# Kernel tuning notes

Measured on AMD Instinct MI355X. Metric: run time of the kernel, lower is better.

The kernel has to match this reference:

```python
import jax, jax.numpy as jnp
import numpy as np

B, N, H, HEADS, L = 8, 64, 512, 8, 4
VOCAB, NBOND, CLS = 128, 8, 2
SP = H // HEADS
SCALE = float(np.sqrt(H))  # module divides by sqrt(hidden_dim), not sqrt(sp_dim)


def _ln(x):
    # fresh nn.LayerNorm each call -> gamma=1, beta=0
    m = jnp.mean(x, -1, keepdims=True)
    v = jnp.mean((x - m) ** 2, -1, keepdims=True)
    return (x - m) / jnp.sqrt(v + 1e-5)


def _split(x):  # [B,N,H] -> [B,h,N,sp]
    return x.reshape(B, N, HEADS, SP).transpose(0, 2, 1, 3)


def setup_inputs() -> dict:
    key = jax.random.key(0)
    ks = jax.random.split(key, 16)
    s = 0.05
    return {
        "input_batch": jax.random.randint(ks[0], (B, N), 0, VOCAB),
        "adj_m": jax.random.randint(ks[1], (B, N, N), 0, NBOND),
        "atom_emb": jax.random.normal(ks[2], (VOCAB, H), jnp.float32) * s,
        "bond_emb": jax.random.normal(ks[3], (NBOND, H), jnp.float32) * s,
        "Wq": jax.random.normal(ks[4], (L, H, H), jnp.float32) * s,
        "Wk": jax.random.normal(ks[5], (L, H, H), jnp.float32) * s,
        "Wv": jax.random.normal(ks[6], (L, H, H), jnp.float32) * s,
        "Wew": jax.random.normal(ks[7], (L, H, H), jnp.float32) * s,
        "Wstack": jax.random.normal(ks[8], (L, H, H), jnp.float32) * s,
        "Wf1": jax.random.normal(ks[9], (L, H, 4 * H), jnp.float32) * s,
        "Wf2": jax.random.normal(ks[10], (L, 4 * H, H), jnp.float32) * s,
        "Wout": jax.random.normal(ks[11], (H, H), jnp.float32) * s,
        "Wpred": jax.random.normal(ks[12], (H, CLS), jnp.float32) * s,
        "bpred": jnp.zeros((CLS,), jnp.float32),
    }


def _forward(input_batch, adj_m, atom_emb, bond_emb, Wq, Wk, Wv, Wew,
             Wstack, Wf1, Wf2, Wout, Wpred, bpred):
    x = atom_emb[input_batch]        # [B,N,H] atom embeddings
    bond = bond_emb[adj_m]           # [B,N,N,H] bond embeddings
    neg = jnp.where(adj_m > 0, 0.0, -jnp.inf)[:, None, :, :]  # [B,1,N,N]
    for l in range(L):
        xn = _ln(x)
        q = _split(xn @ Wq[l])
        k = _split(xn @ Wk[l])
        v = _split(xn @ Wv[l])
        ew = bond @ Wew[l]           # [B,N,N,H]
        w = ew.reshape(B, N, N, HEADS, SP).transpose(0, 3, 1, 2, 4)  # [B,h,N,N,sp]
        # bond_influence==1: sim_ij = q_i . (k_j + w_ij)
        logits = jnp.einsum('bhid,bhjd->bhij', q, k) \
               + jnp.einsum('bhid,bhijd->bhij', q, w)
        attn = jax.nn.softmax(logits / SCALE + neg, axis=-1)
        o = jnp.einsum('bhij,bhjd->bhid', attn, v)
        o = o.transpose(0, 2, 1, 3).reshape(B, N, H) @ Wstack[l]
        attn_resid = o + xn
        ff = jax.nn.relu(_ln(attn_resid) @ Wf1[l]) @ Wf2[l]
        x = ff + attn_resid          # transformer_output
        # edge attention update: softmax over {w.w, w.x_i, w.x_j}
        ew_s = jnp.sum(ew * ew, -1)                      # [B,N,N]
        a0 = jnp.einsum('bijh,bih->bij', ew, x)
        a1 = jnp.einsum('bijh,bjh->bij', ew, x)
        wgt = jax.nn.softmax(jnp.stack([ew_s, a0, a1], -1) / SCALE, -1)  # [B,N,N,3]
        bond = (wgt[..., 0:1] * ew
                + wgt[..., 1:2] * x[:, :, None, :]
                + wgt[..., 2:3] * x[:, None, :, :])      # new edge state
    cls = jnp.tanh(x[:, 0, :] @ Wout)
    return jax.nn.softmax(cls @ Wpred + bpred, axis=-1)


def reference(input_batch, adj_m, atom_emb, bond_emb, Wq, Wk, Wv, Wew,
              Wstack, Wf1, Wf2, Wout, Wpred, bpred):
    return _forward(input_batch, adj_m, atom_emb, bond_emb, Wq, Wk, Wv, Wew,
                    Wstack, Wf1, Wf2, Wout, Wpred, bpred)
```

## Files before the change

### kernel.cpp

```cpp
#include <hip/hip_runtime.h>
#include <hip/hip_bf16.h>

typedef __hip_bfloat16 bf16;

#define B_     8
#define N_     64
#define H_     512
#define HEADS_ 8
#define SP_    64
#define L_     4
static constexpr float INV_SCALE = 0.044194173824159216f;

typedef __attribute__((ext_vector_type(8))) short short8;
typedef __attribute__((ext_vector_type(4))) float f32x4;

__device__ __forceinline__ void unpack8(uint4 u, float* f) {
    f[0] = __uint_as_float(u.x << 16); f[1] = __uint_as_float(u.x & 0xffff0000u);
    f[2] = __uint_as_float(u.y << 16); f[3] = __uint_as_float(u.y & 0xffff0000u);
    f[4] = __uint_as_float(u.z << 16); f[5] = __uint_as_float(u.z & 0xffff0000u);
    f[6] = __uint_as_float(u.w << 16); f[7] = __uint_as_float(u.w & 0xffff0000u);
}

__device__ __forceinline__ bf16 f2bf(float v) { return __float2bfloat16(v); }

// ... 84 lines not shown
                    float v = acc[mt][nt][i];
                    if (EPI == 2) v = fmaxf(v, 0.0f);
                    C[(size_t)row * N + col] = __float2bfloat16(v);
                }
            }
    }
}

template <int EPI, bool SPLIT>
__launch_bounds__(256)
__global__ void mfma_gemm_s(const bf16* __restrict__ A, const bf16* __restrict__ Bt,
                            void* __restrict__ Cv, const float* __restrict__ R,
                            int M, int N, int K) {
    __shared__ __align__(16) char lds[4 * 64 * RSTR];
    int kbeg = 0, kend = K;
    const bf16* B2 = Bt;
    void* C2 = Cv;
    if (SPLIT) {
        int ks = K / gridDim.z;
        kbeg = blockIdx.z * ks;
        kend = kbeg + ks;
        C2 = (void*)((float*)Cv + (size_t)blockIdx.z * M * N);
        gemm64_body<0>(lds, A, B2, C2, nullptr, M, N, K, blockIdx.x, blockIdx.y, kbeg, kend);
    } else {
        B2 = Bt + (size_t)blockIdx.z * N * K;
        if (EPI <= 1) C2 = (void*)((float*)Cv + (size_t)blockIdx.z * M * N);
        gemm64_body<EPI>(lds, A, B2, C2, R, M, N, K, blockIdx.x, blockIdx.y, kbeg, kend);
    }
}


__device__ __forceinline__ void ptable_body(char* lds, const float* __restrict__ q,
        const bf16* __restrict__ Bt, float* __restrict__ P, int b, int h, bool shr) {
    char* As = lds;
    char* Bs = lds + 2 * 64 * RSTR;
    const int tid = threadIdx.x;
    const int w = tid >> 6, lane = tid & 63;
    const int wr = (w >> 1) * 32, wc = (w & 1) * 32;
    const int m0 = lane & 15, q4 = lane >> 4;
    const int rA = tid >> 3;
    const int cA = tid & 7;
    const int ksP = cA >> 2;
    const int cB = (cA & 3) * 16;
    const int cE = cA * 8;

    const float* Aq = q + (size_t)(b * 64) * 512 + h * 64;
    const bf16*  Bb = Bt + (shr ? (size_t)0 : (size_t)b * 64 * 512) + h * 64;

    float4 fa0 = *(const float4*)(Aq + (size_t)rA * 512 + cE);
    float4 fa1 = *(const float4*)(Aq + (size_t)rA * 512 + cE + 4);
    float4 fb0 = *(const float4*)(Aq + (size_t)(rA + 32) * 512 + cE);
    float4 fb1 = *(const float4*)(Aq + (size_t)(rA + 32) * 512 + cE + 4);
    uint4 bv0 = *(const uint4*)(Bb + (size_t)rA * 512 + cE);
    uint4 bv1 = *(const uint4*)(Bb + (size_t)(rA + 32) * 512 + cE);
    uint4 av0 = pack8bf(fa0, fa1);
    uint4 av1 = pack8bf(fb0, fb1);
    *(uint4*)(As + ksP * (64 * RSTR) + rA * RSTR + cB) = av0;
    *(uint4*)(As + ksP * (64 * RSTR) + (rA + 32) * RSTR + cB) = av1;
    *(uint4*)(Bs + ksP * (64 * RSTR) + rA * RSTR + cB) = bv0;
    *(uint4*)(Bs + ksP * (64 * RSTR) + (rA + 32) * RSTR + cB) = bv1;
    __syncthreads();

    f32x4 acc[2][2] = {};
    short8 af[2][2], bfr[2][2];
    #pragma unroll
    for (int ks = 0; ks < 2; ++ks)
        #pragma unroll
        for (int t = 0; t < 2; ++t) {
            af[ks][t]  = *(const short8*)(As + ks * (64 * RSTR) + (wr + t * 16 + m0) * RSTR + q4 * 16);
            bfr[ks][t] = *(const short8*)(Bs + ks * (64 * RSTR) + (wc + t * 16 + m0) * RSTR + q4 * 16);
        }
    #pragma unroll
    for (int ks = 0; ks < 2; ++ks)
        #pragma unroll
        for (int mt = 0; mt < 2; ++mt)
            #pragma unroll
            for (int nt = 0; nt < 2; ++nt)
                acc[mt][nt] = __builtin_amdgcn_mfma_f32_16x16x32_bf16(
                    af[ks][mt], bfr[ks][nt], acc[mt][nt], 0, 0, 0);

    #pragma unroll
    for (int mt = 0; mt < 2; ++mt)
        #pragma unroll
        for (int i = 0; i < 4; ++i) {
            int row = wr + mt * 16 + q4 * 4 + i;
            #pragma unroll
            for (int nt = 0; nt < 2; ++nt) {
                int col = wc + nt * 16 + m0;
                P[(((size_t)b * 8 + h) * 64 + row) * 64 + col] = acc[mt][nt][i];
            }
        }
}

__device__ __forceinline__ void ugemm_body(char* lds, const float* __restrict__ q,
        const bf16* __restrict__ wc3, bf16* __restrict__ ubf, int h, int mb, int nb) {
    char* As = lds;
    char* Bs = lds + 2 * 64 * RSTR;
    const int tid = threadIdx.x;
    const int w = tid >> 6, lane = tid & 63;
    const int wr = (w >> 1) * 32, wc = (w & 1) * 32;
    const int m0 = lane & 15, q4 = lane >> 4;
    const int rA = tid >> 3;
    const int cA = tid & 7;
    const int ksP = cA >> 2;
    const int cB = (cA & 3) * 16;
    const int cE = cA * 8;

    const float* Aq = q + (size_t)(mb * 64) * 512 + h * 64;
    const bf16*  Bt = wc3 + (size_t)(nb * 64) * 512 + h * 64;

    float4 fa0 = *(const float4*)(Aq + (size_t)rA * 512 + cE);
    float4 fa1 = *(const float4*)(Aq + (size_t)rA * 512 + cE + 4);
    float4 fb0 = *(const float4*)(Aq + (size_t)(rA + 32) * 512 + cE);
    float4 fb1 = *(const float4*)(Aq + (size_t)(rA + 32) * 512 + cE + 4);
    uint4 b0 = *(const uint4*)(Bt + (size_t)rA * 512 + cE);
    uint4 b1 = *(const uint4*)(Bt + (size_t)(rA + 32) * 512 + cE);
    uint4 a0 = pack8bf(fa0, fa1);
    uint4 a1 = pack8bf(fb0, fb1);
    *(uint4*)(As + ksP * (64 * RSTR) + rA * RSTR + cB) = a0;
    *(uint4*)(As + ksP * (64 * RSTR) + (rA + 32) * RSTR + cB) = a1;
    *(uint4*)(Bs + ksP * (64 * RSTR) + rA * RSTR + cB) = b0;
    *(uint4*)(Bs + ksP * (64 * RSTR) + (rA + 32) * RSTR + cB) = b1;
    __syncthreads();

    f32x4 acc[2][2] = {};
    short8 af[2][2], bfr[2][2];
    #pragma unroll
    for (int ks = 0; ks < 2; ++ks)
        #pragma unroll
        for (int t = 0; t < 2; ++t) {
            af[ks][t]  = *(const short8*)(As + ks * (64 * RSTR) + (wr + t * 16 + m0) * RSTR + q4 * 16);
            bfr[ks][t] = *(const short8*)(Bs + ks * (64 * RSTR) + (wc + t * 16 + m0) * RSTR + q4 * 16);
        }
    #pragma unroll
    for (int ks = 0; ks < 2; ++ks)
        #pragma unroll
        for (int mt = 0; mt < 2; ++mt)
            #pragma unroll
            for (int nt = 0; nt < 2; ++nt)
                acc[mt][nt] = __builtin_amdgcn_mfma_f32_16x16x32_bf16(
                    af[ks][mt], bfr[ks][nt], acc[mt][nt], 0, 0, 0);

    #pragma unroll
    for (int mt = 0; mt < 2; ++mt)
        #pragma unroll
        for (int i = 0; i < 4; ++i) {
            int row = mb * 64 + wr + mt * 16 + q4 * 4 + i;
            #pragma unroll
            for (int nt = 0; nt < 2; ++nt) {
                int col = nb * 64 + wc + nt * 16 + m0;
                ubf[(size_t)row * 4096 + h * 512 + col] = f2bf(acc[mt][nt][i]);
            }
        }
}

__device__ __forceinline__ void coeff1_body(const int* __restrict__ adj,
        const float* __restrict__ c0a, const float* __restrict__ c1a, const float* __restrict__ c2a,
        const float* __restrict__ gbuf, int row, int j,
        float* __restrict__ w0o, float* __restrict__ w1o, float* __restrict__ w2o) {
    int b = row >> 6, i = row & 63;
    int p = row * 64 + j;
    int t = adj[p];
    const float* TXX = gbuf + 0 * 32768 + (size_t)b * 4096;
    const float* TEX = gbuf + 1 * 32768 + (size_t)b * 4096;
    const float* TXx = gbuf + 2 * 32768 + (size_t)b * 4096;
    const float* TEx = gbuf + 3 * 32768 + (size_t)b * 4096;
    const float* TEE = gbuf + 4 * 32768 + (size_t)b * 4096;
    float c0 = c0a[p], c1 = c1a[p], c2 = c2a[p];
    float s1 = c0 * TEx[t * 64 + i] + c1 * TXx[i * 64 + i] + c2 * TXx[j * 64 + i];
    float s2 = c0 * TEx[t * 64 + j] + c1 * TXx[i * 64 + j] + c2 * TXx[j * 64 + j];
    float s0 = c0 * c0 * TEE[t * 64 + t] + c1 * c1 * TXX[i * 64 + i] + c2 * c2 * TXX[j * 64 + j]
             + 2.f * c0 * c1 * TEX[t * 64 + i] + 2.f * c0 * c2 * TEX[t * 64 + j]
             + 2.f * c1 * c2 * TXX[i * 64 + j];
    float t0 = s0 * INV_SCALE, t1 = s1 * INV_SCALE, t2 = s2 * INV_SCALE;
    float m = fmaxf(t0, fmaxf(t1, t2));
    float e0 = expf(t0 - m), e1 = expf(t1 - m), e2 = expf(t2 - m);
    float inv = 1.0f / (e0 + e1 + e2);
    w0o[p] = e0 * inv;
    w1o[p] = e1 * inv;
    w2o[p] = e2 * inv;
}

__device__ __forceinline__ void coeff2_body(const int* __restrict__ adj,
        const float* __restrict__ c0a, const float* __restrict__ c1a, const float* __restrict__ c2a,
        const float* __restrict__ c0b, const float* __restrict__ c1b, const float* __restrict__ c2b,
        const float* __restrict__ gbuf, int row, int j,
        float* __restrict__ w0o, float* __restrict__ w1o, float* __restrict__ w2o) {
    int b = row >> 6, i = row & 63;
    int p = row * 64 + j;
    int t = adj[p];
    const float* TXX = gbuf + 0 * 32768 + (size_t)b * 4096;
    const float* TXY = gbuf + 1 * 32768 + (size_t)b * 4096;
    const float* TYY = gbuf + 2 * 32768 + (size_t)b * 4096;
    const float* TEX = gbuf + 3 * 32768 + (size_t)b * 4096;
    const float* TEY = gbuf + 4 * 32768 + (size_t)b * 4096;
    const float* TEE = gbuf + 5 * 32768 + (size_t)b * 4096;
    const float* TXx = gbuf + 6 * 32768 + (size_t)b * 4096;
    const float* TYx = gbuf + 7 * 32768 + (size_t)b * 4096;
    const float* TEx = gbuf + 8 * 32768 + (size_t)b * 4096;
    float a0 = c0b[p];
    float AE = a0 * c0a[p], Aa = a0 * c1a[p], Ab = a0 * c2a[p];
    float Ac = c1b[p], Ad = c2b[p];
    float s1 = AE * TEx[t * 64 + i] + Aa * TXx[i * 64 + i] + Ab * TXx[j * 64 + i]
             + Ac * TYx[i * 64 + i] + Ad * TYx[j * 64 + i];
    float s2 = AE * TEx[t * 64 + j] + Aa * TXx[i * 64 + j] + Ab * TXx[j * 64 + j]
             + Ac * TYx[i * 64 + j] + Ad * TYx[j * 64 + j];
    float s0 = AE * AE * TEE[t * 64 + t] + Aa * Aa * TXX[i * 64 + i] + Ab * Ab * TXX[j * 64 + j]
             + Ac * Ac * TYY[i * 64 + i] + Ad * Ad * TYY[j * 64 + j]
             + 2.f * AE * Aa * TEX[t * 64 + i] + 2.f * AE * Ab * TEX[t * 64 + j]
             + 2.f * AE * Ac * TEY[t * 64 + i] + 2.f * AE * Ad * TEY[t * 64 + j]
             + 2.f * Aa * Ab * TXX[i * 64 + j]
             + 2.f * Aa * Ac * TXY[i * 64 + i] + 2.f * Aa * Ad * TXY[i * 64 + j]
             + 2.f * Ab * Ac * TXY[j * 64 + i] + 2.f * Ab * Ad * TXY[j * 64 + j]
             + 2.f * Ac * Ad * TYY[i * 64 + j];
    float t0 = s0 * INV_SCALE, t1 = s1 * INV_SCALE, t2 = s2 * INV_SCALE;
    float m = fmaxf(t0, fmaxf(t1, t2));
    float e0 = expf(t0 - m), e1 = expf(t1 - m), e2 = expf(t2 - m);
    float inv = 1.0f / (e0 + e1 + e2);
    w0o[p] = e0 * inv;
    w1o[p] = e1 * inv;
    w2o[p] = e2 * inv;
}

__launch_bounds__(256)
__global__ void setup_kernel(const int* __restrict__ ids, const float* __restrict__ atom_emb,
                             const float* __restrict__ bond_emb,
                             const float* __restrict__ Wq, const float* __restrict__ Wk,
                             const float* __restrict__ Wv, const float* __restrict__ Wew,
                             const float* __restrict__ Wst,
                             const float* __restrict__ Wf1, const float* __restrict__ Wf2,
                             float* __restrict__ xn, bf16* __restrict__ xn_bf,
                             bf16* __restrict__ qkvt, bf16* __restrict__ ewt,
                             bf16* __restrict__ stackt,
                             bf16* __restrict__ f1t, bf16* __restrict__ f2t,
                             bf16* __restrict__ bond_bf, bf16* __restrict__ wc3) {
    __shared__ __align__(16) float smem[64 * 65];
    const size_t KN = (size_t)H_ * H_;
    int bid = blockIdx.x;
    int tid = threadIdx.x;

    if (bid < 512) {
        int row = bid;
        const float* r = atom_emb + (size_t)ids[row] * H_;
        float x0 = r[tid], x1 = r[tid + 256];
        float s = x0 + x1, sq = x0 * x0 + x1 * x1;
        #pragma unroll
        for (int off = 32; off; off >>= 1) {
            s  += __shfl_xor(s,  off);
            sq += __shfl_xor(sq, off);
        }
        int w = tid >> 6;
        if ((tid & 63) == 0) { smem[w] = s; smem[4 + w] = sq; }
        __syncthreads();
        float S = smem[0] + smem[1] + smem[2] + smem[3];
        float Q = smem[4] + smem[5] + smem[6] + smem[7];
        float mean = S * (1.0f / H_);
        float var  = Q * (1.0f / H_) - mean * mean;
        float inv  = rsqrtf(var + 1e-5f);
        float y0 = (x0 - mean) * inv, y1 = (x1 - mean) * inv;
        xn[(size_t)row * H_ + tid]       = y0;
        xn[(size_t)row * H_ + tid + 256] = y1;
        xn_bf[(size_t)row * H_ + tid]       = f2bf(y0);
        xn_bf[(size_t)row * H_ + tid + 256] = f2bf(y1);
    } else if (bid < 3840) {
        const float* W; bf16* Wt; int K, N, kb, nb;
        if (bid < 1792) {
            int idx = bid - 512;
            int z = idx >> 6, rem = idx & 63;
            kb = rem & 7; nb = rem >> 3;
            K = 512; N = 512;
            if (z < 12) {
                int sss = z >> 2, l = z & 3;
                W  = (sss == 0 ? Wq : sss == 1 ? Wk : Wv) + (size_t)l * KN;
                Wt = qkvt + (size_t)l * 3 * KN + (size_t)sss * KN;
            } else if (z < 16) {
                int l = z - 12;
                W = Wew + (size_t)l * KN; Wt = ewt + (size_t)l * KN;
            } else {
                int l = z - 16;
                W = Wst + (size_t)l * KN; Wt = stackt + (size_t)l * KN;
            }
        } else {
            int idx = bid - 1792;
            int z = idx >> 8;
            int idx2 = idx & 255;
            const size_t KN4 = (size_t)4 * H_ * H_;
            if (z < 4) {
                W = Wf1 + (size_t)z * KN4; Wt = f1t + (size_t)z * KN4; K = 512; N = 2048;
                kb = idx2 & 7; nb = idx2 >> 3;
            } else {
                W = Wf2 + (size_t)(z - 4) * KN4; Wt = f2t + (size_t)(z - 4) * KN4; K = 2048; N = 512;
                kb = idx2 >> 3; nb = idx2 & 7;
            }
        }
        int k0 = kb * 64, n0 = nb * 64;
        float (*tt)[65] = (float(*)[65])smem;
        int rr = tid >> 4, c4 = (tid & 15) * 4;
        #pragma unroll
        for (int it = 0; it < 4; ++it) {
            float4 v = *(const float4*)(W + (size_t)(k0 + rr + it * 16) * N + n0 + c4);
            tt[rr + it * 16][c4 + 0] = v.x;
            tt[rr + it * 16][c4 + 1] = v.y;
            tt[rr + it * 16][c4 + 2] = v.z;
            tt[rr + it * 16][c4 + 3] = v.w;
        }
        __syncthreads();
        int nr = tid >> 3, k8 = (tid & 7) * 8;
        #pragma unroll
        for (int it = 0; it < 2; ++it) {
            int nn = nr + it * 32;
            __align__(16) bf16 ob[8];
            #pragma unroll
            for (int e = 0; e < 8; ++e)
                ob[e] = f2bf(tt[k8 + e][nn]);
            *(uint4*)(Wt + (size_t)(n0 + nn) * K + k0 + k8) = *(const uint4*)ob;
        }
    } else if (bid < 3968) {
        int idx = bid - 3840;
        int t = idx >> 1;
        int c = (idx & 1) * 256 + tid;
        bond_bf[t * 512 + c] = (t < 8) ? f2bf(bond_emb[t * 512 + c]) : f2bf(0.0f);
    } else {
        int idx = bid - 3968;
        int gid = idx * 256 + tid;
        const float4* p = (const float4*)(Wew + 3 * KN + (size_t)gid * 8);
        float4 a = p[0], b = p[1];
        *(uint4*)(wc3 + (size_t)gid * 8) = pack8bf(a, b);
    }
}

__launch_bounds__(256)
__global__ void qkv0_e0(const bf16* __restrict__ xn_bf, const bf16* __restrict__ qkvt,
                        float* __restrict__ qkv,
                        const bf16* __restrict__ bond_bf, const bf16* __restrict__ ewt0,
                        bf16* __restrict__ E0) {
    __shared__ __align__(16) char lds[4 * 64 * RSTR];
    int bid = blockIdx.x;
    if (bid < 192) {
        int z = bid >> 6, rem = bid & 63;
        int mb = rem >> 3, by = rem & 7;
        gemm64_body<0>(lds, xn_bf, qkvt + (size_t)z * 262144,
                       qkv + (size_t)z * 262144, nullptr, 512, 512, 512, mb, by, 0, 512);
    } else {
        gemm64_body<3>(lds, bond_bf, ewt0, E0, nullptr, 64, 512, 512,
                       0, bid - 192, 0, 512);
    }
}

__launch_bounds__(256)
__global__ void basis1_qkv_ec(const bf16* __restrict__ x_bf, const bf16* __restrict__ E0,
                              const bf16* __restrict__ ewt1,
                              bf16* __restrict__ xw1, bf16* __restrict__ e0w1,
                              const bf16* __restrict__ xn_bf, const bf16* __restrict__ qkvt_l,
                              float* __restrict__ qkv,
                              const int* __restrict__ adj, const float* __restrict__ x,
                              float* __restrict__ w0o, float* __restrict__ w1o,
                              float* __restrict__ w2o) {
    __shared__ __align__(16) char lds[4 * 64 * RSTR];
    int bid = blockIdx.x;
    if (bid < 264) {
        int bx = bid >> 3, by = bid & 7;
        if (bx < 8)
            gemm64_body<3>(lds, x_bf, ewt1, xw1, nullptr, 512, 512, 512, bx, by, 0, 512);
        else if (bx == 8)
            gemm64_body<3>(lds, E0, ewt1, e0w1, nullptr, 64, 512, 512, 0, by, 0, 512);
        else {
            int tq = bx - 9;
            int z = tq >> 3, mb = tq & 7;
            gemm64_body<0>(lds, xn_bf, qkvt_l + (size_t)z * 262144,
                           qkv + (size_t)z * 262144, nullptr, 512, 512, 512, mb, by, 0, 512);
        }
    } else {
        int k = bid - 264;
        int tid = threadIdx.x;
        int lane = tid & 63, tyv = tid >> 6;
        for (int pp = 0; pp < 4; ++pp) {
            int pair = k * 16 + pp * 4 + tyv;
            int b = pair >> 12;
            int i = (pair >> 6) & 63;
            int j = pair & 63;
            const uint4*  e4  = (const uint4*)(E0 + (size_t)adj[pair] * H_);
            const float4* xi4 = (const float4*)(x + (size_t)(b * 64 + i) * H_);
            const float4* xj4 = (const float4*)(x + (size_t)(b * 64 + j) * H_);
            uint4  eu = e4[lane];
            float4 a0 = xi4[lane * 2], a1 = xi4[lane * 2 + 1];
            float4 c0 = xj4[lane * 2], c1 = xj4[lane * 2 + 1];
            float ef[8], af[8], cf[8];
            unpack8(eu, ef);
            af[0] = a0.x; af[1] = a0.y; af[2] = a0.z; af[3] = a0.w;
            af[4] = a1.x; af[5] = a1.y; af[6] = a1.z; af[7] = a1.w;
            cf[0] = c0.x; cf[1] = c0.y; cf[2] = c0.z; cf[3] = c0.w;
            cf[4] = c1.x; cf[5] = c1.y; cf[6] = c1.z; cf[7] = c1.w;
            float s0 = 0.f, s1 = 0.f, s2 = 0.f;
            #pragma unroll
            for (int t = 0; t < 8; ++t) {
                s0 += ef[t] * ef[t]; s1 += ef[t] * af[t]; s2 += ef[t] * cf[t];
            }
            #pragma unroll
            for (int off = 32; off; off >>= 1) {
                s0 += __shfl_xor(s0, off);
                s1 += __shfl_xor(s1, off);
                s2 += __shfl_xor(s2, off);
            }
            float t0 = s0 * INV_SCALE, t1 = s1 * INV_SCALE, t2 = s2 * INV_SCALE;
            float m = fmaxf(t0, fmaxf(t1, t2));
            float e0 = expf(t0 - m), e1 = expf(t1 - m), e2 = expf(t2 - m);
            float inv = 1.0f / (e0 + e1 + e2);
            if (lane == 0) {
                w0o[pair] = e0 * inv;
                w1o[pair] = e1 * inv;
                w2o[pair] = e2 * inv;
            }
        }
    }
}

__launch_bounds__(256)
__global__ void basis2_qkv_g1(const bf16* __restrict__ xw1, const bf16* __restrict__ x_bf,
                              const bf16* __restrict__ e0w1, const bf16* __restrict__ ewt2,
                              bf16* __restrict__ xw12, bf16* __restrict__ x2w2,
                              bf16* __restrict__ e0w12,
                              const bf16* __restrict__ xn_bf, const bf16* __restrict__ qkvt_l,
                              float* __restrict__ qkv, float* __restrict__ gbuf) {
    __shared__ __align__(16) char lds[4 * 64 * RSTR];
    int bid = blockIdx.x;
    if (bid < 328) {
        int bx = bid >> 3, by = bid & 7;
        if (bx < 8)
            gemm64_body<3>(lds, xw1, ewt2, xw12, nullptr, 512, 512, 512, bx, by, 0, 512);
        else if (bx < 16)
            gemm64_body<3>(lds, x_bf, ewt2, x2w2, nullptr, 512, 512, 512, bx - 8, by, 0, 512);
        else if (bx == 16)
            gemm64_body<3>(lds, e0w1, ewt2, e0w12, nullptr, 64, 512, 512, 0, by, 0, 512);
        else {
            int tq = bx - 17;
            int z = tq >> 3, mb = tq & 7;
            gemm64_body<0>(lds, xn_bf, qkvt_l + (size_t)z * 262144,
                           qkv + (size_t)z * 262144, nullptr, 512, 512, 512, mb, by, 0, 512);
        }
    } else {
        int k = bid - 328;
        int b = k & 7, z = k >> 3;
        size_t ob = (size_t)b * 32768;
        const bf16 *A, *Bt;
        switch (z) {
            case 0: A = xw1 + ob; Bt = xw1 + ob; break;
            case 1: A = e0w1;     Bt = xw1 + ob; break;
            case 2: A = xw1 + ob; Bt = x_bf + ob; break;
            case 3: A = e0w1;     Bt = x_bf + ob; break;
            default: A = e0w1;    Bt = e0w1;     break;
        }
        float* C = gbuf + (size_t)z * 32768 + (size_t)b * 4096;
        gemm64_body<0>(lds, A, Bt, C, nullptr, 64, 64, 512, 0, 0, 0, 512);
    }
}

__launch_bounds__(256)
__global__ void ptable2c(const float* __restrict__ q,
                         const bf16* __restrict__ B0, const bf16* __restrict__ B1,
                         const bf16* __restrict__ B2,
                         float* __restrict__ P0, float* __restrict__ P1,
                         float* __restrict__ P2,
                         const int* __restrict__ adj,
                         const float* __restrict__ c0a, const float* __restrict__ c1a,
                         const float* __restrict__ c2a, const float* __restrict__ gbuf,
                         float* __restrict__ w0o, float* __restrict__ w1o,
                         float* __restrict__ w2o) {
    __shared__ __align__(16) char lds[4 * 64 * RSTR];
    int bid = blockIdx.x;
    if (bid < 192) {
        int z = bid >> 6, rem = bid & 63;
        int b = rem >> 3, h = rem & 7;
        const bf16* Bt = (z == 0) ? B0 : (z == 1 ? B1 : B2);
        float* P = (z == 0) ? P0 : (z == 1 ? P1 : P2);
        ptable_body(lds, q, Bt, P, b, h, z == 2);
    } else {
        int k = bid - 192;
        int tid = threadIdx.x;
        int j = tid & 63;
        #pragma unroll
        for (int pass = 0; pass < 2; ++pass) {
            int row = k * 8 + pass * 4 + (tid >> 6);
            coeff1_body(adj, c0a, c1a, c2a, gbuf, row, j, w0o, w1o, w2o);
        }
    }
}

__launch_bounds__(256)
__global__ void ptable_kernel(const float* __restrict__ q,
                              const bf16* __restrict__ B0, const bf16* __restrict__ B1,
                              float* __restrict__ P0, float* __restrict__ P1) {
    __shared__ __align__(16) char lds[4 * 64 * RSTR];
    const int b = blockIdx.x, h = blockIdx.y, z = blockIdx.z;
    const bf16* Bt = (z == 0) ? B0 : B1;
    float* P = (z == 0) ? P0 : P1;
    ptable_body(lds, q, Bt, P, b, h, z == 1);
}

__launch_bounds__(256)
__global__ void l3qkv_g2(const bf16* __restrict__ xn_bf, const bf16* __restrict__ qkvt_l,
                         float* __restrict__ qkv,
                         const bf16* __restrict__ xw12, const bf16* __restrict__ x2w2,
                         const bf16* __restrict__ e0w12, const bf16* __restrict__ x_bf,
                         float* __restrict__ gbuf) {
    __shared__ __align__(16) char lds[4 * 64 * RSTR];
    int bid = blockIdx.x;
    if (bid < 192) {
        int z = bid >> 6, rem = bid & 63;
        int mb = rem >> 3, by = rem & 7;
        gemm64_body<0>(lds, xn_bf, qkvt_l + (size_t)z * 262144,
                       qkv + (size_t)z * 262144, nullptr, 512, 512, 512, mb, by, 0, 512);
    } else {
        int k = bid - 192;
        int b = k & 7, z = k >> 3;
        size_t ob = (size_t)b * 32768;
        const bf16 *A, *Bt;
        switch (z) {
            case 0: A = xw12 + ob; Bt = xw12 + ob; break;
            case 1: A = xw12 + ob; Bt = x2w2 + ob; break;
            case 2: A = x2w2 + ob; Bt = x2w2 + ob; break;
            case 3: A = e0w12;     Bt = xw12 + ob; break;
            case 4: A = e0w12;     Bt = x2w2 + ob; break;
            case 5: A = e0w12;     Bt = e0w12;     break;
            case 6: A = xw12 + ob; Bt = x_bf + ob; break;
            case 7: A = x2w2 + ob; Bt = x_bf + ob; break;
            default: A = e0w12;    Bt = x_bf + ob; break;
        }
        float* C = gbuf + (size_t)z * 32768 + (size_t)b * 4096;
        gemm64_body<0>(lds, A, Bt, C, nullptr, 64, 64, 512, 0, 0, 0, 512);
    }
}

__launch_bounds__(256)
__global__ void u_c2(const float* __restrict__ q, const bf16* __restrict__ wc3,
                     bf16* __restrict__ ubf,
                     const int* __restrict__ adj,
                     const float* __restrict__ c0a, const float* __restrict__ c1a,
                     const float* __restrict__ c2a,
                     const float* __restrict__ c0b, const float* __restrict__ c1b,
                     const float* __restrict__ c2b,
                     const float* __restrict__ gbuf,
                     float* __restrict__ w0o, float* __restrict__ w1o,
                     float* __restrict__ w2o) {
    __shared__ __align__(16) char lds[4 * 64 * RSTR];
    int bid = blockIdx.x;
    if (bid < 512) {
        int h = bid >> 6, mb = (bid >> 3) & 7, nb = bid & 7;
        ugemm_body(lds, q, wc3, ubf, h, mb, nb);
    } else {
        int k = bid - 512;
        int tid = threadIdx.x;
        int j = tid & 63;
        #pragma unroll
        for (int pass = 0; pass < 2; ++pass) {
            int row = k * 8 + pass * 4 + (tid >> 6);
            coeff2_body(adj, c0a, c1a, c2a, c0b, c1b, c2b, gbuf, row, j, w0o, w1o, w2o);
        }
    }
}

__launch_bounds__(256)
__global__ void mbuf_gemm(const bf16* __restrict__ ubf, const bf16* __restrict__ xw12,
                          const bf16* __restrict__ x2w2, const bf16* __restrict__ x_bf,
                          const bf16* __restrict__ e0w12,
                          float* __restrict__ MX, float* __restrict__ MY,
                          float* __restrict__ MZ, float* __restrict__ DE) {
    __shared__ __align__(16) char lds[4 * 64 * RSTR];
    int b = blockIdx.x, mt = blockIdx.y, z = blockIdx.z;
    const bf16* A = ubf + (size_t)b * 512 * 512;
    const bf16* Bt;
    float* C;
    if (z == 0)      { Bt = xw12 + (size_t)b * 64 * 512; C = MX + (size_t)b * 512 * 64; }
    else if (z == 1) { Bt = x2w2 + (size_t)b * 64 * 512; C = MY + (size_t)b * 512 * 64; }
    else if (z == 2) { Bt = x_bf + (size_t)b * 64 * 512; C = MZ + (size_t)b * 512 * 64; }
    else             { Bt = e0w12;                        C = DE + (size_t)b * 512 * 64; }
    gemm64_body<0>(lds, A, Bt, C, nullptr, 512, 64, 512, mt, 0, 0, 512);
}

__global__ void reduce_stack_ln(const float* __restrict__ part, const float* __restrict__ base,
                                float* __restrict__ resid, bf16* __restrict__ ffin_bf) {
    const int MN = 512 * H_;
    int row = blockIdx.x;
    int tid = threadIdx.x;
    size_t b0 = (size_t)row * H_;
    float v0 = base[b0 + tid], v1 = base[b0 + tid + 256];
    #pragma unroll
    for (int s = 0; s < 4; ++s) {
        v0 += part[(size_t)s * MN + b0 + tid];
        v1 += part[(size_t)s * MN + b0 + tid + 256];
    }
    resid[b0 + tid] = v0;
    resid[b0 + tid + 256] = v1;
    float s = v0 + v1, sq = v0 * v0 + v1 * v1;
    #pragma unroll
    for (int off = 32; off; off >>= 1) {
        s  += __shfl_xor(s,  off);
        sq += __shfl_xor(sq, off);
    }
    __shared__ float ls[4], lq[4];
    int w = tid >> 6;
    if ((tid & 63) == 0) { ls[w] = s; lq[w] = sq; }
    __syncthreads();
    float S = ls[0] + ls[1] + ls[2] + ls[3];
    float Q = lq[0] + lq[1] + lq[2] + lq[3];
    float mean = S * (1.0f / H_);
    float var  = Q * (1.0f / H_) - mean * mean;
    float inv  = rsqrtf(var + 1e-5f);
    ffin_bf[b0 + tid]       = f2bf((v0 - mean) * inv);
    ffin_bf[b0 + tid + 256] = f2bf((v1 - mean) * inv);
}

template <bool DO_LN>
__global__ void reduce_ln_kernel(const float* __restrict__ part, const float* __restrict__ resid,
                                 float* __restrict__ x, bf16* __restrict__ x_bf,
                                 float* __restrict__ xn, bf16* __restrict__ xn_bf) {
    const int MN = 512 * H_;
    int row = blockIdx.x;
    int tid = threadIdx.x;
    size_t base = (size_t)row * H_;
    float v0 = resid[base + tid], v1 = resid[base + tid + 256];
    #pragma unroll
    for (int s = 0; s < 4; ++s) {
        v0 += part[(size_t)s * MN + base + tid];
        v1 += part[(size_t)s * MN + base + tid + 256];
    }
    x[base + tid] = v0;
    x[base + tid + 256] = v1;
    x_bf[base + tid]       = f2bf(v0);
    x_bf[base + tid + 256] = f2bf(v1);
    if (DO_LN) {
        float s = v0 + v1, sq = v0 * v0 + v1 * v1;
        #pragma unroll
        for (int off = 32; off; off >>= 1) {
            s  += __shfl_xor(s,  off);
            sq += __shfl_xor(sq, off);
        }
        __shared__ float ls[4], lq[4];
        int w = tid >> 6;
        if ((tid & 63) == 0) { ls[w] = s; lq[w] = sq; }
        __syncthreads();
        float S = ls[0] + ls[1] + ls[2] + ls[3];
        float Q = lq[0] + lq[1] + lq[2] + lq[3];
        float mean = S * (1.0f / H_);
        float var  = Q * (1.0f / H_) - mean * mean;
        float inv  = rsqrtf(var + 1e-5f);
        float y0 = (v0 - mean) * inv, y1 = (v1 - mean) * inv;
        xn[base + tid]       = y0;
        xn[base + tid + 256] = y1;
        xn_bf[base + tid]       = f2bf(y0);
// ... 167 lines not shown
    for (int off = 32; off; off >>= 1) m = fmaxf(m, __shfl_xor(m, off));
    float pe = expf(logit - m);
    float s = pe;
    #pragma unroll
    for (int off = 32; off; off >>= 1) s += __shfl_xor(s, off);
    as[ty][lane] = pe / s;
    __syncthreads();

    const float* vbase = v + (size_t)(b * 64) * H_ + h * 64;
    float oacc = 0.f;
    int d = lane;
    #pragma unroll 8
    for (int jj = 0; jj < 64; ++jj)
        oacc += as[ty][jj] * vbase[(size_t)jj * H_ + d];
    o[(size_t)bi * H_ + h * 64 + d] = __float2bfloat16(oacc);
}

__global__ void cls_part_kernel(const float* __restrict__ x, const float* __restrict__ Wout,
                                float* __restrict__ clspart) {
    int b  = blockIdx.x;
    int cb = blockIdx.y;
    int ks = blockIdx.z;
    int tid = threadIdx.x;
    int c  = cb * 64 + (tid & 63);
    int kk = tid >> 6;
    const float* xr = x + (size_t)(b * 64) * H_;
    int h0 = ks * 128 + kk * 32;
    float acc = 0.f;
    #pragma unroll
    for (int h = 0; h < 32; ++h)
        acc += xr[h0 + h] * Wout[(size_t)(h0 + h) * H_ + c];
    __shared__ float red[4][64];
    red[kk][tid & 63] = acc;
    __syncthreads();
    if (tid < 64) {
        float v = red[0][tid] + red[1][tid] + red[2][tid] + red[3][tid];
        clspart[((size_t)ks * 8 + b) * H_ + cb * 64 + tid] = v;
    }
}

__global__ void cls_pred2_kernel(const float* __restrict__ clspart,
                                 const float* __restrict__ Wpred,
                                 const float* __restrict__ bpred,
                                 float* __restrict__ out) {
    int b = blockIdx.x;
    int tid = threadIdx.x;
    __shared__ float red0[4], red1[4];
    float a0 = 0.f, a1 = 0.f;
    #pragma unroll
    for (int t = 0; t < 2; ++t) {
        int c = tid + t * 256;
        float v = clspart[((size_t)0 * 8 + b) * H_ + c]
                + clspart[((size_t)1 * 8 + b) * H_ + c]
                + clspart[((size_t)2 * 8 + b) * H_ + c]
                + clspart[((size_t)3 * 8 + b) * H_ + c];
        float tv = tanhf(v);
        a0 += tv * Wpred[c * 2 + 0];
        a1 += tv * Wpred[c * 2 + 1];
    }
    #pragma unroll
    for (int off = 32; off; off >>= 1) {
        a0 += __shfl_xor(a0, off);
        a1 += __shfl_xor(a1, off);
    }
    int w = tid >> 6;
    if ((tid & 63) == 0) { red0[w] = a0; red1[w] = a1; }
    __syncthreads();
    if (tid == 0) {
        float s0 = red0[0] + red0[1] + red0[2] + red0[3] + bpred[0];
        float s1 = red1[0] + red1[1] + red1[2] + red1[3] + bpred[1];
        float m = fmaxf(s0, s1);
        float e0 = expf(s0 - m), e1 = expf(s1 - m);
        float inv = 1.0f / (e0 + e1);
        out[b * 2 + 0] = e0 * inv;
        out[b * 2 + 1] = e1 * inv;
    }
}

extern "C" void kernel_launch(void* const* d_in, const int* in_sizes, int n_in,
                              void* d_out, int out_size, void* d_ws, size_t ws_size,
                              hipStream_t stream) {
    const int*   ids      = (const int*)d_in[0];
    const int*   adj      = (const int*)d_in[1];
    const float* atom_emb = (const float*)d_in[2];
    const float* bond_emb = (const float*)d_in[3];
    const float* Wq     = (const float*)d_in[4];
    const float* Wk     = (const float*)d_in[5];
    const float* Wv     = (const float*)d_in[6];
    const float* Wew    = (const float*)d_in[7];
    const float* Wstack = (const float*)d_in[8];
    const float* Wf1    = (const float*)d_in[9];
    const float* Wf2    = (const float*)d_in[10];
    const float* Wout   = (const float*)d_in[11];
    const float* Wpred  = (const float*)d_in[12];
    const float* bpred  = (const float*)d_in[13];

    char* ws = (char*)d_ws;
    size_t off = 0;
    auto alloc = [&](size_t bytes) {
        size_t o = off;
        off += (bytes + 255) & ~(size_t)255;
        return o;
    };
    const size_t ROWS  = (size_t)B_ * N_;
    const size_t PAIRS = (size_t)B_ * N_ * N_;
    const size_t KN    = (size_t)H_ * H_;

    float* x       = (float*)(ws + alloc(ROWS * H_ * 4));
    float* xn      = (float*)(ws + alloc(ROWS * H_ * 4));
    bf16*  xn_bf   = (bf16*) (ws + alloc(ROWS * H_ * 2));
    bf16*  x_bf    = (bf16*) (ws + alloc(ROWS * H_ * 2));
    float* qkv     = (float*)(ws + alloc(3 * ROWS * H_ * 4));
    bf16*  o_bf    = (bf16*) (ws + alloc(ROWS * H_ * 2));
    float* resid   = (float*)(ws + alloc(ROWS * H_ * 4));
    bf16*  ffin_bf = (bf16*) (ws + alloc(ROWS * H_ * 2));
    bf16*  ffh_bf  = (bf16*) (ws + alloc(ROWS * 4 * H_ * 2));
    float* part    = (float*)(ws + alloc(4 * ROWS * H_ * 4));
    float* clspart = (float*)(ws + alloc(4 * 8 * H_ * 4));
    bf16*  ubf     = (bf16*) (ws + alloc(ROWS * 8 * 512 * 2));
    float* MX      = (float*)(ws + alloc((size_t)4096 * 64 * 4));
    float* MY      = (float*)(ws + alloc((size_t)4096 * 64 * 4));
    float* MZ      = (float*)(ws + alloc((size_t)4096 * 64 * 4));
    float* DE      = (float*)(ws + alloc((size_t)4096 * 64 * 4));
    float* PT0     = (float*)(ws + alloc((size_t)4096 * 64 * 4));
    float* PT1     = (float*)(ws + alloc((size_t)4096 * 64 * 4));
    float* PT2     = (float*)(ws + alloc((size_t)4096 * 64 * 4));
    float* gbuf    = (float*)(ws + alloc((size_t)9 * 8 * 4096 * 4));
    bf16*  wc3     = (bf16*) (ws + alloc(KN * 2));
    bf16*  bond_bf = (bf16*) (ws + alloc(64 * H_ * 2));
    bf16*  E0      = (bf16*) (ws + alloc(64 * H_ * 2));
    bf16*  e0w1    = (bf16*) (ws + alloc(64 * H_ * 2));
    bf16*  e0w12   = (bf16*) (ws + alloc(64 * H_ * 2));
    bf16*  xw1     = (bf16*) (ws + alloc(KN * 2));
    bf16*  xw12    = (bf16*) (ws + alloc(KN * 2));
    bf16*  x2w2    = (bf16*) (ws + alloc(KN * 2));
    float* cw      = (float*)(ws + alloc(9 * PAIRS * 4));
    bf16*  qkvt    = (bf16*) (ws + alloc((size_t)L_ * 3 * KN * 2));
    bf16*  ewt     = (bf16*) (ws + alloc((size_t)L_ * KN * 2));
    bf16*  stackt  = (bf16*) (ws + alloc((size_t)L_ * KN * 2));
    bf16*  f1t     = (bf16*) (ws + alloc((size_t)L_ * 4 * KN * 2));
    bf16*  f2t     = (bf16*) (ws + alloc((size_t)L_ * 4 * KN * 2));
    (void)ws_size;

    float* cw0a = cw;
    float* cw1a = cw + PAIRS;
    float* cw2a = cw + 2 * PAIRS;
    float* cw0b = cw + 3 * PAIRS;
    float* cw1b = cw + 4 * PAIRS;
    float* cw2b = cw + 5 * PAIRS;
    float* cw0c = cw + 6 * PAIRS;
    float* cw1c = cw + 7 * PAIRS;
    float* cw2c = cw + 8 * PAIRS;

    setup_kernel<<<4096, 256, 0, stream>>>(ids, atom_emb, bond_emb,
                                           Wq, Wk, Wv, Wew, Wstack, Wf1, Wf2,
                                           xn, xn_bf, qkvt, ewt, stackt, f1t, f2t,
                                           bond_bf, wc3);

    for (int l = 0; l < L_; ++l) {
        if (l == 0) {
            qkv0_e0<<<200, 256, 0, stream>>>(xn_bf, qkvt, qkv, bond_bf, ewt, E0);
            attn_kernel<true><<<dim3(512, 2), dim3(64, 4), 0, stream>>>(qkv, E0, adj, o_bf);
        } else if (l == 1) {
            basis1_qkv_ec<<<2312, 256, 0, stream>>>(
                x_bf, E0, ewt + KN, xw1, e0w1, xn_bf, qkvt + (size_t)3 * KN, qkv,
                adj, x, cw0a, cw1a, cw2a);
            ptable_kernel<<<dim3(8, 8, 2), 256, 0, stream>>>(qkv, xw1, e0w1, PT0, PT1);
            attn13_kernel<1><<<dim3(512, 2), dim3(64, 4), 0, stream>>>(
                qkv, adj, cw0a, cw1a, cw2a, nullptr, nullptr, nullptr,
                PT0, nullptr, PT1, o_bf);
        } else if (l == 2) {
            basis2_qkv_g1<<<368, 256, 0, stream>>>(
                xw1, x_bf, e0w1, ewt + 2 * KN, xw12, x2w2, e0w12,
                xn_bf, qkvt + (size_t)6 * KN, qkv, gbuf);
            ptable2c<<<256, 256, 0, stream>>>(
                qkv, xw12, x2w2, e0w12, PT0, PT1, PT2,
                adj, cw0a, cw1a, cw2a, gbuf, cw0b, cw1b, cw2b);
            attn13_kernel<2><<<dim3(512, 2), dim3(64, 4), 0, stream>>>(
                qkv, adj, cw0a, cw1a, cw2a, cw0b, cw1b, cw2b,
                PT0, PT1, PT2, o_bf);
        } else {
            l3qkv_g2<<<264, 256, 0, stream>>>(
                xn_bf, qkvt + (size_t)9 * KN, qkv, xw12, x2w2, e0w12, x_bf, gbuf);
            u_c2<<<576, 256, 0, stream>>>(
                qkv, wc3, ubf, adj, cw0a, cw1a, cw2a, cw0b, cw1b, cw2b,
                gbuf, cw0c, cw1c, cw2c);
            mbuf_gemm<<<dim3(8, 8, 4), 256, 0, stream>>>(ubf, xw12, x2w2, x_bf, e0w12,
                                                         MX, MY, MZ, DE);
            attn3s2_kernel<<<dim3(512, 2), dim3(64, 4), 0, stream>>>(
                qkv, adj, cw0a, cw1a, cw2a, cw0b, cw1b, cw2b, cw0c, cw1c, cw2c,
                MX, MY, MZ, DE, o_bf);
        }

        mfma_gemm_s<0, true><<<dim3(8, 8, 4), 256, 0, stream>>>(
            o_bf, stackt + (size_t)l * KN, part, nullptr, 512, 512, 512);
        reduce_stack_ln<<<512, 256, 0, stream>>>(part, xn, resid, ffin_bf);
        mfma_gemm_s<2, false><<<dim3(8, 32), 256, 0, stream>>>(
            ffin_bf, f1t + (size_t)l * 4 * KN, ffh_bf, nullptr, 512, 2048, 512);
        mfma_gemm_s<0, true><<<dim3(8, 8, 4), 256, 0, stream>>>(
            ffh_bf, f2t + (size_t)l * 4 * KN, part, nullptr, 512, 512, 2048);
        if (l < L_ - 1)
            reduce_ln_kernel<true><<<512, 256, 0, stream>>>(part, resid, x, x_bf, xn, xn_bf);
        else
            reduce_ln_kernel<false><<<512, 256, 0, stream>>>(part, resid, x, x_bf, xn, xn_bf);
    }

    cls_part_kernel<<<dim3(8, 8, 4), 256, 0, stream>>>(x, Wout, clspart);
    cls_pred2_kernel<<<8, 256, 0, stream>>>(clspart, Wpred, bpred, (float*)d_out);
}
```

Baseline: 345.9 us.

## Compute layer-1 edge softmax coefficients from small Gram tables instead of per-pair dots

The layer-1 edge-update coefficients were computed by a 2048-block path that, for every (b,i,j) pair, took 512-wide dot products of the bond embedding with itself and with x_i and x_j. Those dots now come from small Gram tables: E0·x per batch and E0·E0 across the bond types, built as extra 64x64 GEMM blocks in the basis/QKV kernel. A lightweight coeff0 pass merged into the ptable launch looks them up. Separately, each setup weight-transpose block now handles two tiles, cutting the setup grid from 4096 to 2432 blocks. The trade-off is an added dependency on gbuf Gram results and bf16 Gram products in place of fp32 dot products.

```diff
diff --git a/kernel.cpp b/kernel.cpp
--- a/kernel.cpp
+++ b/kernel.cpp
@@ -260,6 +260,26 @@
                 ubf[(size_t)row * 4096 + h * 512 + col] = f2bf(acc[mt][nt][i]);
             }
         }
+}
+
+__device__ __forceinline__ void coeff0_body(const int* __restrict__ adj,
+        const float* __restrict__ gbuf, int row, int j,
+        float* __restrict__ w0o, float* __restrict__ w1o, float* __restrict__ w2o) {
+    int b = row >> 6, i = row & 63;
+    int p = row * 64 + j;
+    int t = adj[p];
+    const float* G0  = gbuf + 5 * 32768 + (size_t)b * 4096;
+    const float* TEE = gbuf + 6 * 32768;
+    float s0 = TEE[t * 64 + t];
+    float s1 = G0[t * 64 + i];
+    float s2 = G0[t * 64 + j];
+    float t0 = s0 * INV_SCALE, t1 = s1 * INV_SCALE, t2 = s2 * INV_SCALE;
+    float m = fmaxf(t0, fmaxf(t1, t2));
+    float e0 = expf(t0 - m), e1 = expf(t1 - m), e2 = expf(t2 - m);
+    float inv = 1.0f / (e0 + e1 + e2);
+    w0o[p] = e0 * inv;
+    w1o[p] = e1 * inv;
+    w2o[p] = e2 * inv;
 }
 
 __device__ __forceinline__ void coeff1_body(const int* __restrict__ adj,
@@ -370,66 +390,69 @@
         xn[(size_t)row * H_ + tid + 256] = y1;
         xn_bf[(size_t)row * H_ + tid]       = f2bf(y0);
         xn_bf[(size_t)row * H_ + tid + 256] = f2bf(y1);
-    } else if (bid < 3840) {
-        const float* W; bf16* Wt; int K, N, kb, nb;
-        if (bid < 1792) {
-            int idx = bid - 512;
-            int z = idx >> 6, rem = idx & 63;
-            kb = rem & 7; nb = rem >> 3;
-            K = 512; N = 512;
-            if (z < 12) {
-                int sss = z >> 2, l = z & 3;
-                W  = (sss == 0 ? Wq : sss == 1 ? Wk : Wv) + (size_t)l * KN;
-                Wt = qkvt + (size_t)l * 3 * KN + (size_t)sss * KN;
-            } else if (z < 16) {
-                int l = z - 12;
-                W = Wew + (size_t)l * KN; Wt = ewt + (size_t)l * KN;
+    } else if (bid < 2176) {
+        for (int sub = 0; sub < 2; ++sub) {
+            const float* W; bf16* Wt; int K, N, kb, nb;
+            if (bid < 1152) {
+                int idx = (bid - 512) * 2 + sub;
+                int z = idx >> 6, rem = idx & 63;
+                kb = rem & 7; nb = rem >> 3;
+                K = 512; N = 512;
+                if (z < 12) {
+                    int sss = z >> 2, l = z & 3;
+                    W  = (sss == 0 ? Wq : sss == 1 ? Wk : Wv) + (size_t)l * KN;
+                    Wt = qkvt + (size_t)l * 3 * KN + (size_t)sss * KN;
+                } else if (z < 16) {
+                    int l = z - 12;
+                    W = Wew + (size_t)l * KN; Wt = ewt + (size_t)l * KN;
+                } else {
+                    int l = z - 16;
+                    W = Wst + (size_t)l * KN; Wt = stackt + (size_t)l * KN;
+                }
             } else {
-                int l = z - 16;
-                W = Wst + (size_t)l * KN; Wt = stackt + (size_t)l * KN;
+                int idx = (bid - 1152) * 2 + sub;
+                int z = idx >> 8;
+                int idx2 = idx & 255;
+                const size_t KN4 = (size_t)4 * H_ * H_;
+                if (z < 4) {
+                    W = Wf1 + (size_t)z * KN4; Wt = f1t + (size_t)z * KN4; K = 512; N = 2048;
+                    kb = idx2 & 7; nb = idx2 >> 3;
+                } else {
+                    W = Wf2 + (size_t)(z - 4) * KN4; Wt = f2t + (size_t)(z - 4) * KN4; K = 2048; N = 512;
+                    kb = idx2 >> 3; nb = idx2 & 7;
+                }
             }
-        } else {
-            int idx = bid - 1792;
-            int z = idx >> 8;
-            int idx2 = idx & 255;
-            const size_t KN4 = (size_t)4 * H_ * H_;
-            if (z < 4) {
-                W = Wf1 + (size_t)z * KN4; Wt = f1t + (size_t)z * KN4; K = 512; N = 2048;
-                kb = idx2 & 7; nb = idx2 >> 3;
-            } else {
-                W = Wf2 + (size_t)(z - 4) * KN4; Wt = f2t + (size_t)(z - 4) * KN4; K = 2048; N = 512;
-                kb = idx2 >> 3; nb = idx2 & 7;
+            int k0 = kb * 64, n0 = nb * 64;
+            float (*tt)[65] = (float(*)[65])smem;
+            int rr = tid >> 4, c4 = (tid & 15) * 4;
+            if (sub) __syncthreads();
+            #pragma unroll
+            for (int it = 0; it < 4; ++it) {
+                float4 v = *(const float4*)(W + (size_t)(k0 + rr + it * 16) * N + n0 + c4);
+                tt[rr + it * 16][c4 + 0] = v.x;
+                tt[rr + it * 16][c4 + 1] = v.y;
+                tt[rr + it * 16][c4 + 2] = v.z;
+                tt[rr + it * 16][c4 + 3] = v.w;
             }
-        }
-        int k0 = kb * 64, n0 = nb * 64;
-        float (*tt)[65] = (float(*)[65])smem;
-        int rr = tid >> 4, c4 = (tid & 15) * 4;
-        #pragma unroll
-        for (int it = 0; it < 4; ++it) {
-            float4 v = *(const float4*)(W + (size_t)(k0 + rr + it * 16) * N + n0 + c4);
-            tt[rr + it * 16][c4 + 0] = v.x;
-            tt[rr + it * 16][c4 + 1] = v.y;
-            tt[rr + it * 16][c4 + 2] = v.z;
-            tt[rr + it * 16][c4 + 3] = v.w;
-        }
-        __syncthreads();
-        int nr = tid >> 3, k8 = (tid & 7) * 8;
-        #pragma unroll
-        for (int it = 0; it < 2; ++it) {
-            int nn = nr + it * 32;
-            __align__(16) bf16 ob[8];
+            __syncthreads();
+            int nr = tid >> 3, k8 = (tid & 7) * 8;
             #pragma unroll
-            for (int e = 0; e < 8; ++e)
-                ob[e] = f2bf(tt[k8 + e][nn]);
-            *(uint4*)(Wt + (size_t)(n0 + nn) * K + k0 + k8) = *(const uint4*)ob;
-        }
-    } else if (bid < 3968) {
-        int idx = bid - 3840;
+            for (int it = 0; it < 2; ++it) {
+                int nn = nr + it * 32;
+                __align__(16) bf16 ob[8];
+                #pragma unroll
+                for (int e = 0; e < 8; ++e)
+                    ob[e] = f2bf(tt[k8 + e][nn]);
+                *(uint4*)(Wt + (size_t)(n0 + nn) * K + k0 + k8) = *(const uint4*)ob;
+            }
+        }
+    } else if (bid < 2304) {
+        int idx = bid - 2176;
         int t = idx >> 1;
         int c = (idx & 1) * 256 + tid;
         bond_bf[t * 512 + c] = (t < 8) ? f2bf(bond_emb[t * 512 + c]) : f2bf(0.0f);
     } else {
-        int idx = bid - 3968;
+        int idx = bid - 2304;
         int gid = idx * 256 + tid;
         const float4* p = (const float4*)(Wew + 3 * KN + (size_t)gid * 8);
         float4 a = p[0], b = p[1];
@@ -456,14 +479,11 @@
 }
 
 __launch_bounds__(256)
-__global__ void basis1_qkv_ec(const bf16* __restrict__ x_bf, const bf16* __restrict__ E0,
+__global__ void basis1_qkv_g0(const bf16* __restrict__ x_bf, const bf16* __restrict__ E0,
                               const bf16* __restrict__ ewt1,
                               bf16* __restrict__ xw1, bf16* __restrict__ e0w1,
                               const bf16* __restrict__ xn_bf, const bf16* __restrict__ qkvt_l,
-                              float* __restrict__ qkv,
-                              const int* __restrict__ adj, const float* __restrict__ x,
-                              float* __restrict__ w0o, float* __restrict__ w1o,
-                              float* __restrict__ w2o) {
+                              float* __restrict__ qkv, float* __restrict__ gbuf) {
     __shared__ __align__(16) char lds[4 * 64 * RSTR];
     int bid = blockIdx.x;
     if (bid < 264) {
@@ -478,47 +498,40 @@
             gemm64_body<0>(lds, xn_bf, qkvt_l + (size_t)z * 262144,
                            qkv + (size_t)z * 262144, nullptr, 512, 512, 512, mb, by, 0, 512);
         }
+    } else if (bid < 272) {
+        int b = bid - 264;
+        gemm64_body<0>(lds, E0, x_bf + (size_t)b * 32768,
+                       gbuf + 5 * 32768 + (size_t)b * 4096, nullptr,
+                       64, 64, 512, 0, 0, 0, 512);
     } else {
-        int k = bid - 264;
+        gemm64_body<0>(lds, E0, E0, gbuf + 6 * 32768, nullptr,
+                       64, 64, 512, 0, 0, 0, 512);
+    }
+}
+
+__launch_bounds__(256)
+__global__ void ptable1c(const float* __restrict__ q,
+                         const bf16* __restrict__ B0, const bf16* __restrict__ B1,
+                         float* __restrict__ P0, float* __restrict__ P1,
+                         const int* __restrict__ adj, const float* __restrict__ gbuf,
+                         float* __restrict__ w0o, float* __restrict__ w1o,
+                         float* __restrict__ w2o) {
+    __shared__ __align__(16) char lds[4 * 64 * RSTR];
+    int bid = blockIdx.x;
+    if (bid < 128) {
+        int z = bid >> 6, rem = bid & 63;
+        int b = rem >> 3, h = rem & 7;
+        const bf16* Bt = (z == 0) ? B0 : B1;
+        float* P = (z == 0) ? P0 : P1;
+        ptable_body(lds, q, Bt, P, b, h, z == 1);
+    } else {
+        int k = bid - 128;
         int tid = threadIdx.x;
-        int lane = tid & 63, tyv = tid >> 6;
-        for (int pp = 0; pp < 4; ++pp) {
-            int pair = k * 16 + pp * 4 + tyv;
-            int b = pair >> 12;
-            int i = (pair >> 6) & 63;
-            int j = pair & 63;
-            const uint4*  e4  = (const uint4*)(E0 + (size_t)adj[pair] * H_);
-            const float4* xi4 = (const float4*)(x + (size_t)(b * 64 + i) * H_);
-            const float4* xj4 = (const float4*)(x + (size_t)(b * 64 + j) * H_);
-            uint4  eu = e4[lane];
-            float4 a0 = xi4[lane * 2], a1 = xi4[lane * 2 + 1];
-            float4 c0 = xj4[lane * 2], c1 = xj4[lane * 2 + 1];
-            float ef[8], af[8], cf[8];
-            unpack8(eu, ef);
-            af[0] = a0.x; af[1] = a0.y; af[2] = a0.z; af[3] = a0.w;
-            af[4] = a1.x; af[5] = a1.y; af[6] = a1.z; af[7] = a1.w;
-            cf[0] = c0.x; cf[1] = c0.y; cf[2] = c0.z; cf[3] = c0.w;
-            cf[4] = c1.x; cf[5] = c1.y; cf[6] = c1.z; cf[7] = c1.w;
-            float s0 = 0.f, s1 = 0.f, s2 = 0.f;
-            #pragma unroll
-            for (int t = 0; t < 8; ++t) {
-                s0 += ef[t] * ef[t]; s1 += ef[t] * af[t]; s2 += ef[t] * cf[t];
-            }
-            #pragma unroll
-            for (int off = 32; off; off >>= 1) {
-                s0 += __shfl_xor(s0, off);
-                s1 += __shfl_xor(s1, off);
-                s2 += __shfl_xor(s2, off);
-            }
-            float t0 = s0 * INV_SCALE, t1 = s1 * INV_SCALE, t2 = s2 * INV_SCALE;
-            float m = fmaxf(t0, fmaxf(t1, t2));
-            float e0 = expf(t0 - m), e1 = expf(t1 - m), e2 = expf(t2 - m);
-            float inv = 1.0f / (e0 + e1 + e2);
-            if (lane == 0) {
-                w0o[pair] = e0 * inv;
-                w1o[pair] = e1 * inv;
-                w2o[pair] = e2 * inv;
-            }
+        int j = tid & 63;
+        #pragma unroll
+        for (int pass = 0; pass < 2; ++pass) {
+            int row = k * 8 + pass * 4 + (tid >> 6);
+            coeff0_body(adj, gbuf, row, j, w0o, w1o, w2o);
         }
     }
 }
@@ -592,17 +605,6 @@
             coeff1_body(adj, c0a, c1a, c2a, gbuf, row, j, w0o, w1o, w2o);
         }
     }
-}
-
-__launch_bounds__(256)
-__global__ void ptable_kernel(const float* __restrict__ q,
-                              const bf16* __restrict__ B0, const bf16* __restrict__ B1,
-                              float* __restrict__ P0, float* __restrict__ P1) {
-    __shared__ __align__(16) char lds[4 * 64 * RSTR];
-    const int b = blockIdx.x, h = blockIdx.y, z = blockIdx.z;
-    const bf16* Bt = (z == 0) ? B0 : B1;
-    float* P = (z == 0) ? P0 : P1;
-    ptable_body(lds, q, Bt, P, b, h, z == 1);
 }
 
 __launch_bounds__(256)
@@ -1076,7 +1078,7 @@
     float* cw1c = cw + 7 * PAIRS;
     float* cw2c = cw + 8 * PAIRS;
 
-    setup_kernel<<<4096, 256, 0, stream>>>(ids, atom_emb, bond_emb,
+    setup_kernel<<<2432, 256, 0, stream>>>(ids, atom_emb, bond_emb,
                                            Wq, Wk, Wv, Wew, Wstack, Wf1, Wf2,
                                            xn, xn_bf, qkvt, ewt, stackt, f1t, f2t,
                                            bond_bf, wc3);
@@ -1086,10 +1088,10 @@
             qkv0_e0<<<200, 256, 0, stream>>>(xn_bf, qkvt, qkv, bond_bf, ewt, E0);
             attn_kernel<true><<<dim3(512, 2), dim3(64, 4), 0, stream>>>(qkv, E0, adj, o_bf);
         } else if (l == 1) {
-            basis1_qkv_ec<<<2312, 256, 0, stream>>>(
-                x_bf, E0, ewt + KN, xw1, e0w1, xn_bf, qkvt + (size_t)3 * KN, qkv,
-                adj, x, cw0a, cw1a, cw2a);
-            ptable_kernel<<<dim3(8, 8, 2), 256, 0, stream>>>(qkv, xw1, e0w1, PT0, PT1);
+            basis1_qkv_g0<<<273, 256, 0, stream>>>(
+                x_bf, E0, ewt + KN, xw1, e0w1, xn_bf, qkvt + (size_t)3 * KN, qkv, gbuf);
+            ptable1c<<<192, 256, 0, stream>>>(qkv, xw1, e0w1, PT0, PT1,
+                                              adj, gbuf, cw0a, cw1a, cw2a);
             attn13_kernel<1><<<dim3(512, 2), dim3(64, 4), 0, stream>>>(
                 qkv, adj, cw0a, cw1a, cw2a, nullptr, nullptr, nullptr,
                 PT0, nullptr, PT1, o_bf);
```

Result: faster. 338.3 us, median of 2 (-2.2%).
